# Kernel tuning notes

Hardware: AMD Instinct MI355X
Metric: run time of the kernel (lower is better)

## Reference

```python
import jax, jax.numpy as jnp
import numpy as np

NH, HD, MB = 32, 64, 16        # heads, head_dim, TTT mini-batch size
BASE_LR = 1.0
ROPE_THETA = 10000.0


def _ln(x, w, b, eps):
    mu = x.mean(-1, keepdims=True)
    var = ((x - mu) ** 2).mean(-1, keepdims=True)
    return (x - mu) / jnp.sqrt(var + eps) * w + b


def _rotate_half(x):
    x1, x2 = jnp.split(x, 2, axis=-1)
    return jnp.concatenate([-x2, x1], axis=-1)


def _ln_l2_bwd(x, target, g, b, eps=1e-6):
    # grad of ||LN(x)*g+b - target||^2 / 2 wrt x (fused, as in ttt-lm)
    D = x.shape[-1]
    mu = x.mean(-1, keepdims=True)
    var = ((x - mu) ** 2).mean(-1, keepdims=True)
    std = jnp.sqrt(var + eps)
    xh = (x - mu) / std
    gxh = (g * xh + b - target) * g
    return (D * gxh - gxh.sum(-1, keepdims=True) - xh * (gxh * xh).sum(-1, keepdims=True)) / (D * std)


def _ttt_forward(x, q_w, k_w, v_w, o_w, ttt_lr_w, ttt_lr_b, token_idx_off,
                 ttt_norm_w, ttt_norm_b, W1, b1, post_w, post_b):
    B, L, C = x.shape
    NM = L // MB
    XQ = (x @ q_w).reshape(B, L, NH, HD).transpose(0, 2, 1, 3)  # [B,NH,L,HD]
    XK = (x @ k_w).reshape(B, L, NH, HD).transpose(0, 2, 1, 3)
    XV = (x @ v_w).reshape(B, L, NH, HD).transpose(0, 2, 1, 3)
    # rotary embedding at position_ids % mini_batch_size
    pos = (jnp.arange(L) % MB).astype(jnp.float32)
    inv = 1.0 / (ROPE_THETA ** (jnp.arange(0, HD, 2, dtype=jnp.float32) / HD))
    fr = pos[:, None] * inv[None, :]
    emb = jnp.concatenate([fr, fr], axis=-1)           # [L,HD]
    cos, sin = jnp.cos(emb), jnp.sin(emb)
    XQ = XQ * cos + _rotate_half(XQ) * sin
    XK = XK * cos + _rotate_half(XK) * sin
    # learning-rate gate (eta)
    Xm = x.reshape(B, NM, MB, C)
    ttt_lr = jax.nn.sigmoid(jnp.einsum('bnkc,hdc->bhnkd', Xm, ttt_lr_w)
                            + ttt_lr_b.reshape(1, NH, 1, 1, 1))       # [B,NH,NM,MB,1]
    ttt_lr_eta = BASE_LR * ttt_lr.transpose(0, 1, 2, 4, 3) / HD       # [B,NH,NM,1,MB]
    tok = jnp.maximum(1.0 / jnp.arange(1, MB + 1, dtype=jnp.float32) + token_idx_off, 0.0)
    eta = tok.reshape(1, 1, 1, MB, 1) * ttt_lr_eta                    # [B,NH,NM,MB,MB]

    def tomb(t):  # [B,NH,L,HD] -> [NM,B,NH,MB,HD]
        return t.reshape(B, NH, NM, MB, HD).transpose(2, 0, 1, 3, 4)

    xs = (tomb(XQ), tomb(XK), tomb(XV), eta.transpose(2, 0, 1, 3, 4))
    lw = ttt_norm_w.reshape(1, NH, 1, HD)
    lb = ttt_norm_b.reshape(1, NH, 1, HD)
    tril = jnp.tril(jnp.ones((MB, MB), x.dtype))
    W1s = jnp.broadcast_to(W1, (B, NH, HD, HD)).astype(x.dtype)
    b1s = jnp.broadcast_to(b1, (B, NH, 1, HD)).astype(x.dtype)

    def step(carry, xs_t):
        W1c, b1c = carry
        xq, xk, xv, et = xs_t                      # [B,NH,MB,HD], et [B,NH,MB,MB]
        Z1 = xk @ W1c + b1c
        grad = _ln_l2_bwd(Z1, xv - xk, lw, lb)     # grad of per-head TTT loss wrt Z1
        Attn1 = jnp.tril(xq @ xk.transpose(0, 1, 3, 2))
        b1_bar = b1c - (et * tril) @ grad
        Z1_bar = xq @ W1c - (et * Attn1) @ grad + b1_bar
        last_eta = et[:, :, -1, :, None]           # [B,NH,MB,1]
        W1n = W1c - jnp.einsum('bhki,bhkj->bhij', last_eta * xk, grad)
        b1n = b1c - (last_eta * grad).sum(-2, keepdims=True)
        out = xq + _ln(Z1_bar, lw, lb, 1e-6)
        return (W1n, b1n), out

    _, outs = jax.lax.scan(step, (W1s, b1s), xs)   # outs: [NM,B,NH,MB,HD]
    y = outs.transpose(1, 0, 3, 2, 4).reshape(B, L, C)
    y = _ln(y, post_w, post_b, 1e-6)
    return y @ o_w


def setup_inputs() -> dict:
    key = jax.random.key(0)
    ks = jax.random.split(key, 16)
    B, L, C, DH = 4, 2048, 2048, 1024
    s = 0.02
    return {
        'enc_input': jax.random.normal(ks[0], (B, L, C), jnp.float32),
        'ln1_w': jnp.ones((C,), jnp.float32), 'ln1_b': jnp.zeros((C,), jnp.float32),
        'q_w': jax.random.normal(ks[1], (C, C), jnp.float32) * s,
        'k_w': jax.random.normal(ks[2], (C, C), jnp.float32) * s,
        'v_w': jax.random.normal(ks[3], (C, C), jnp.float32) * s,
        'o_w': jax.random.normal(ks[4], (C, C), jnp.float32) * s,
        'ttt_lr_w': jax.random.normal(ks[5], (NH, 1, C), jnp.float32) * s,
        'ttt_lr_b': jax.random.normal(ks[6], (NH,), jnp.float32) * s,
        'token_idx_off': jax.random.normal(ks[7], (MB,), jnp.float32) * 0.01,
        'ttt_norm_w': jnp.ones((NH, HD), jnp.float32),
        'ttt_norm_b': jnp.zeros((NH, HD), jnp.float32),
        'W1': jax.random.normal(ks[8], (NH, HD, HD), jnp.float32) * s,
        'b1': jnp.zeros((NH, 1, HD), jnp.float32),
        'post_w': jnp.ones((C,), jnp.float32), 'post_b': jnp.zeros((C,), jnp.float32),
        'ffn_ln_w': jnp.ones((C,), jnp.float32), 'ffn_ln_b': jnp.zeros((C,), jnp.float32),
        'w1f': jax.random.normal(ks[9], (C, DH), jnp.float32) * s,
        'b1f': jnp.zeros((DH,), jnp.float32),
        'w2f': jax.random.normal(ks[10], (DH, C), jnp.float32) * s,
        'b2f': jnp.zeros((C,), jnp.float32),
    }


def reference(enc_input, ln1_w, ln1_b, q_w, k_w, v_w, o_w, ttt_lr_w, ttt_lr_b,
              token_idx_off, ttt_norm_w, ttt_norm_b, W1, b1, post_w, post_b,
              ffn_ln_w, ffn_ln_b, w1f, b1f, w2f, b2f):
    # pre-LN (torch default eps=1e-5) + TTT linear block + residual
    x = _ln(enc_input, ln1_w, ln1_b, 1e-5)
    y = _ttt_forward(x, q_w, k_w, v_w, o_w, ttt_lr_w, ttt_lr_b, token_idx_off,
                     ttt_norm_w, ttt_norm_b, W1, b1, post_w, post_b)
    y = y + enc_input
    # position-wise FFN (pre-LN eps=1e-6) + residual; dropout = eval no-op
    z = _ln(y, ffn_ln_w, ffn_ln_b, 1e-6)
    z = jax.nn.relu(z @ w1f + b1f) @ w2f + b2f
    return z + y
```

## Files before the change

### kernel.cpp

```cpp
#include <hip/hip_runtime.h>

typedef unsigned short u16;
typedef __attribute__((ext_vector_type(8))) short short8;
typedef __attribute__((ext_vector_type(8))) unsigned short ushort8;
typedef __attribute__((ext_vector_type(4))) float f32x4;
typedef __attribute__((ext_vector_type(2))) float f32x2;

#define DEV __device__ __forceinline__

DEV float bf2f(u16 u){ union{unsigned int i; float f;} v; v.i = ((unsigned int)u)<<16u; return v.f; }
DEV u16 f2bf(float f){ union{float f; unsigned int i;} v; v.f=f; unsigned int r = v.i + 0x7FFFu + ((v.i>>16)&1u); return (u16)(r>>16); }

DEV void gload16(const u16* g, u16* l){
  __builtin_amdgcn_global_load_lds((const __attribute__((address_space(1))) void*)g,
                                   (__attribute__((address_space(3))) void*)l, 16, 0, 0);
}

DEV float wsum(float v){
  v += __shfl_xor(v, 32, 64);
  v += __shfl_xor(v, 16, 64);
  v += __shfl_xor(v, 8, 64);
  v += __shfl_xor(v, 4, 64);
  v += __shfl_xor(v, 2, 64);
  v += __shfl_xor(v, 1, 64);
  return v;
}
DEV float qsum(float v){
  v += __shfl_xor(v, 16, 64);
  v += __shfl_xor(v, 32, 64);
  return v;
}
DEV float jsum(float v){
  v += __shfl_xor(v, 1, 64);
  v += __shfl_xor(v, 2, 64);
  v += __shfl_xor(v, 4, 64);
  v += __shfl_xor(v, 8, 64);
  return v;
}

DEV float block_sum(float v, float* red){
  v = wsum(v);
  __syncthreads();
  if((threadIdx.x & 63u)==0) red[threadIdx.x>>6] = v;
  __syncthreads();
  return red[0]+red[1]+red[2]+red[3];
}

#define BARS() do{ asm volatile("s_waitcnt lgkmcnt(0)" ::: "memory"); \
  __builtin_amdgcn_s_barrier(); __builtin_amdgcn_sched_barrier(0); }while(0)

__global__ __launch_bounds__(256) void ln_row(
    const float* __restrict__ in, const float* __restrict__ w, const float* __restrict__ bb,
    float eps, u16* __restrict__ outb)
{
  __shared__ float red[4];
  const int row = blockIdx.x, t = threadIdx.x;
  const float* p = in + (size_t)row*2048 + t*8;
  f32x4 a = *(const f32x4*)p;
  f32x4 c = *(const f32x4*)(p+4);
  float s = a[0]+a[1]+a[2]+a[3]+c[0]+c[1]+c[2]+c[3];
  s = block_sum(s, red);
  float mu = s*(1.f/2048.f);
  float vs = 0.f;
  #pragma unroll
  for(int j=0;j<4;j++){ float d=a[j]-mu; vs += d*d; }
  #pragma unroll
  for(int j=0;j<4;j++){ float d=c[j]-mu; vs += d*d; }
  vs = block_sum(vs, red);
  float rstd = rsqrtf(vs*(1.f/2048.f) + eps);
  f32x4 w0 = *(const f32x4*)(w + t*8);
  f32x4 w1 = *(const f32x4*)(w + t*8 + 4);
  f32x4 b0 = *(const f32x4*)(bb + t*8);
  f32x4 b1 = *(const f32x4*)(bb + t*8 + 4);
  ushort8 o;
  #pragma unroll
  for(int j=0;j<4;j++) o[j]   = f2bf((a[j]-mu)*rstd*w0[j] + b0[j]);
  #pragma unroll
  for(int j=0;j<4;j++) o[j+4] = f2bf((c[j]-mu)*rstd*w1[j] + b1[j]);
  *(ushort8*)(outb + (size_t)row*2048 + t*8) = o;
}

__global__ __launch_bounds__(256) void transpose_cast(
    const float* __restrict__ src, u16* __restrict__ dst, int K, int N)
{
  __shared__ float tile[32][33];
  const int kb = blockIdx.x*32, nb = blockIdx.y*32;
  const int tx = threadIdx.x & 31, ty = threadIdx.x >> 5;
  #pragma unroll
  for(int i=0;i<4;i++){
    int k = ty + i*8;
    tile[k][tx] = src[(size_t)(kb+k)*N + nb + tx];
  }
  __syncthreads();
  #pragma unroll
  for(int i=0;i<4;i++){
    int nn = ty + i*8;
    dst[(size_t)(nb+nn)*K + kb + tx] = f2bf(tile[tx][nn]);
  }
}

__global__ __launch_bounds__(256) void cast_lrw(const float* __restrict__ lrw, u16* __restrict__ dst)
{
  int i = blockIdx.x*256 + threadIdx.x;
  if (i < 32*2048) dst[i] = f2bf(lrw[i]);
  else dst[i] = 0;
}

__global__ void rope_init(const float* __restrict__ tio, float* __restrict__ cosb,
                          float* __restrict__ sinb, float* __restrict__ tokb)
{
  int t = blockIdx.x*256 + threadIdx.x;
  if (t < 1024){
    int p = t>>6, d = t&63;
    float inv = powf(10000.f, -(float)(2*(d&31))/64.f);
    float fr = (float)p * inv;
    cosb[t] = cosf(fr);
    sinb[t] = sinf(fr);
  }
  if (blockIdx.x==0 && threadIdx.x<16)
    tokb[threadIdx.x] = fmaxf(1.f/(float)(threadIdx.x+1) + tio[threadIdx.x], 0.f);
}

#define MM(MI,NI,AA,BB) acc[MI][NI] = __builtin_amdgcn_mfma_f32_16x16x32_bf16(AA, BB, acc[MI][NI], 0, 0, 0)

#define RD_A(D,KH,MF) (*(const short8*)(ldsb + ((D)<<16) + ((KH)<<14) + (wm<<13) + ((MF)<<10) + loff))
#define RD_B(D,KH,NF) (*(const short8*)(ldsb + ((D)<<16) + 32768 + ((KH)<<14) + (wn<<12) + ((NF)<<10) + loff))

#define PHASE(D,KH,MH,RB,STG,VM) { \
  __builtin_amdgcn_sched_barrier(0); \
  if (RB){ b0 = RD_B(D,KH,0); b1 = RD_B(D,KH,1); b2 = RD_B(D,KH,2); b3 = RD_B(D,KH,3); } \
  short8 a0 = RD_A(D,KH,4*(MH)+0); \
  short8 a1 = RD_A(D,KH,4*(MH)+1); \
  short8 a2 = RD_A(D,KH,4*(MH)+2); \
  short8 a3 = RD_A(D,KH,4*(MH)+3); \
  STG; \
  __builtin_amdgcn_sched_barrier(0); \
  __builtin_amdgcn_s_barrier(); \
  asm volatile("s_waitcnt lgkmcnt(0)" ::: "memory"); \
  __builtin_amdgcn_sched_barrier(0); \
  __builtin_amdgcn_s_setprio(1); \
  MM(4*(MH)+0,0,a0,b0); MM(4*(MH)+1,0,a1,b0); MM(4*(MH)+2,0,a2,b0); MM(4*(MH)+3,0,a3,b0); \
  MM(4*(MH)+0,1,a0,b1); MM(4*(MH)+1,1,a1,b1); MM(4*(MH)+2,1,a2,b1); MM(4*(MH)+3,1,a3,b1); \
  MM(4*(MH)+0,2,a0,b2); MM(4*(MH)+1,2,a1,b2); MM(4*(MH)+2,2,a2,b2); MM(4*(MH)+3,2,a3,b2); \
  MM(4*(MH)+0,3,a0,b3); MM(4*(MH)+1,3,a1,b3); MM(4*(MH)+2,3,a2,b3); MM(4*(MH)+3,3,a3,b3); \
  __builtin_amdgcn_s_setprio(0); \
  if (VM){ asm volatile("s_waitcnt vmcnt(8)" ::: "memory"); } \
  __builtin_amdgcn_sched_barrier(0); \
  __builtin_amdgcn_s_barrier(); \
}

template<int EPI>
__global__ __launch_bounds__(512, 2) void gemm256(
    const u16* __restrict__ A, const u16* __restrict__ Bt,
    float* __restrict__ C, u16* __restrict__ Cb,
    const float* __restrict__ bias, const float* __restrict__ resid,
    int Nld, int Nreal, int K, int ntN)
{
  extern __shared__ u16 lds[];
  const int t = threadIdx.x, lane = t&63, wv = t>>6;
  const int wm = wv>>2, wn = wv&3;
  const int fr = lane&15, kq = lane>>4;

  int bid = blockIdx.x;
  {
    int nwg = gridDim.x;
    int q = nwg>>3, r = nwg&7;
    int x = bid&7, l = bid>>3;
    bid = (x<r) ? (x*(q+1)+l) : (r*(q+1)+(x-r)*q+l);
  }
  const int bm = bid/ntN, bn = bid%ntN;

  f32x4 acc[8][4];
  #pragma unroll
  for(int i=0;i<8;i++)
    #pragma unroll
    for(int j=0;j<4;j++) acc[i][j]=(f32x4){0.f,0.f,0.f,0.f};

  const u16* gA = A  + (size_t)(bm*256)*K;
  const u16* gB = Bt + (size_t)(bn*256)*K;

  const int Ls   = (t&7) ^ ((t>>3)&7);
  const int rstg = ((t>>3)<<1) | (Ls>>2);
  const int cstg = (Ls&3)<<3;
  u16* const ldsw = lds + (wv<<9);

  const int Plane = (((fr&1)<<2) | kq) ^ (fr>>1);
  const int loff  = ((fr>>1)<<7) | (Plane<<4);
  const char* const ldsb = (const char*)lds;

  auto stA = [&](int d, int kh, int kts){
    u16* lb = ldsw + (d<<15) + (kh<<13);
    const u16* g = gA + (size_t)rstg*K + kts + (kh<<5) + cstg;
    gload16(g, lb);
    gload16(g + ((size_t)K<<7), lb + 4096);
  };
  auto stB = [&](int d, int kh, int kts){
    u16* lb = ldsw + (d<<15) + 16384 + (kh<<13);
    const u16* g = gB + (size_t)rstg*K + kts + (kh<<5) + cstg;
    gload16(g, lb);
    gload16(g + ((size_t)K<<7), lb + 4096);
  };

  stA(0,0,0); stB(0,0,0); stA(0,1,0); stB(0,1,0); stA(1,0,64); stB(1,0,64);
  asm volatile("s_waitcnt vmcnt(8)" ::: "memory");
  __builtin_amdgcn_sched_barrier(0);
  __builtin_amdgcn_s_barrier();

  for (int kt = 0; kt < K; kt += 128){
    const int ktp = (kt+128 < K) ? kt+128 : 0;
    const int ktq = (kt+192 < K) ? kt+192 : kt+192-K;
    short8 b0={0},b1={0},b2={0},b3={0};
    PHASE(0,0,0,1, stA(1,1,kt+64), 0)
    PHASE(0,0,1,0, stB(1,1,kt+64), 1)
    PHASE(0,1,0,1, stA(0,0,ktp),   0)
    PHASE(0,1,1,0, stB(0,0,ktp),   1)
    PHASE(1,0,0,1, stA(0,1,ktp),   0)
    PHASE(1,0,1,0, stB(0,1,ktp),   1)
    PHASE(1,1,0,1, stA(1,0,ktq),   0)
    PHASE(1,1,1,0, stB(1,0,ktq),   1)
  }

  const int cr = (lane>>4)<<2, cc = lane&15;
  #pragma unroll
  for(int mi=0;mi<8;mi++){
    #pragma unroll
    for(int ni=0;ni<4;ni++){
      const int row0 = bm*256 + wm*128 + mi*16 + cr;
      const int col  = bn*256 + wn*64  + ni*16 + cc;
      if (col < Nreal){
        #pragma unroll
        for(int rr=0;rr<4;rr++){
          size_t idx = (size_t)(row0+rr)*Nld + col;
          float v = acc[mi][ni][rr];
          if (EPI==1 || EPI==3) v += resid[idx];
          if (EPI==2 || EPI==3) v += bias[col];
          if (EPI==2){ v = fmaxf(v, 0.f); Cb[idx] = f2bf(v); }
          else if (EPI==4){ Cb[idx] = f2bf(v); }
          else C[idx] = v;
        }
      }
    }
  }
}

#define W1LD 72
#define XLD  72
#define GTLD 40
#define EKLD 40
#define EALD 40
#define TLD  17

__global__ __launch_bounds__(512, 1) void ttt_scan(
    const u16* __restrict__ XQKV,
    const float* __restrict__ ropec, const float* __restrict__ ropes,
    const float* __restrict__ tokp,
    const float* __restrict__ nw, const float* __restrict__ nb,
    const float* __restrict__ lrb,
    const float* __restrict__ W1i,
    const float* __restrict__ b1i,
    float* __restrict__ Y)
{
  const int blk = blockIdx.x, b = blk>>5, h = blk&31;
  const int t = threadIdx.x, lane = t&63, wv = t>>6;
  const int fr = lane&15, quad = lane>>4;
  const int i0 = wv*2, i1 = i0+1;

  __shared__ u16 W1bf[64*W1LD];
  __shared__ u16 xqbf[2][16*XLD];
  __shared__ u16 xkbf[2][16*XLD];
  __shared__ u16 exkT[2][64*EKLD];
  __shared__ u16 gradTbf[64*GTLD];
  __shared__ u16 etaA[16*EALD];
  __shared__ float tgT[2][64*TLD];
  __shared__ float xqT[2][64*TLD];
  __shared__ float b1s[64];
  __shared__ f32x2 lwlb[64];
  __shared__ float lrs[2][16];
  __shared__ float tokl[16];

  const float lrbh = lrb[h];
  const float cc0 = ropec[i0*64 + lane], ss0 = ropes[i0*64 + lane];
  const float cc1 = ropec[i1*64 + lane], ss1 = ropes[i1*64 + lane];
  const float tok15 = tokp[15];
  const float ct = tok15*(1.f/64.f);
  const float sg = (lane<32)? -1.f : 1.f;

  const int m0 = (wv*2)>>2,   n0 = (wv*2)&3;
  const int m1 = (wv*2+1)>>2, n1 = (wv*2+1)&3;
  f32x4 wfa, wfb;
  {
    const float* wsrc = W1i + (size_t)h*4096;
    #pragma unroll
    for(int r=0;r<4;r++){
      wfa[r] = wsrc[(n0*16+fr)*64 + (m0*16+quad*4+r)];
      wfb[r] = wsrc[(n1*16+fr)*64 + (m1*16+quad*4+r)];
    }
    #pragma unroll
    for(int r=0;r<4;r++){
      W1bf[(m0*16+quad*4+r)*W1LD + n0*16 + fr] = f2bf(wfa[r]);
      W1bf[(m1*16+quad*4+r)*W1LD + n1*16 + fr] = f2bf(wfb[r]);
    }
  }
  for(int i=t;i<64*24;i+=512){
    int rr=i/24, cp=16+i%24;
    gradTbf[rr*GTLD+cp]=0; exkT[0][rr*EKLD+cp]=0; exkT[1][rr*EKLD+cp]=0;
  }
  for(int i=t;i<16*24;i+=512){ int rr=i/24, cp=16+i%24; etaA[rr*EALD+cp]=0; }
  if (t<64){ b1s[t]=b1i[h*64+t]; lwlb[t]=(f32x2){nw[h*64+t], nb[h*64+t]}; }
  if (t<16) tokl[t]=tokp[t];

  auto stage = [&](int bf, u16 Pq0,u16 Pk0,u16 Pv0,u16 Pl0,
                           u16 Pq1,u16 Pk1,u16 Pv1,u16 Pl1){
    float q0=bf2f(Pq0), k0=bf2f(Pk0), v0=bf2f(Pv0);
    float q1=bf2f(Pq1), k1=bf2f(Pk1), v1=bf2f(Pv1);
    float qr0 = q0*cc0 + sg*__shfl_xor(q0,32,64)*ss0;
    float kr0 = k0*cc0 + sg*__shfl_xor(k0,32,64)*ss0;
    float qr1 = q1*cc1 + sg*__shfl_xor(q1,32,64)*ss1;
    float kr1 = k1*cc1 + sg*__shfl_xor(k1,32,64)*ss1;
    float lr0 = 1.f/(1.f + expf(-(bf2f(Pl0) + lrbh)));
    float lr1 = 1.f/(1.f + expf(-(bf2f(Pl1) + lrbh)));
    xqbf[bf][i0*XLD+lane] = f2bf(qr0);
    xqbf[bf][i1*XLD+lane] = f2bf(qr1);
    xkbf[bf][i0*XLD+lane] = f2bf(kr0);
    xkbf[bf][i1*XLD+lane] = f2bf(kr1);
    exkT[bf][lane*EKLD+i0] = f2bf(-ct*lr0*kr0);
    exkT[bf][lane*EKLD+i1] = f2bf(-ct*lr1*kr1);
    tgT[bf][lane*TLD+i0] = v0 - kr0;
    tgT[bf][lane*TLD+i1] = v1 - kr1;
    xqT[bf][lane*TLD+i0] = qr0;
    xqT[bf][lane*TLD+i1] = qr1;
    if (lane==0){ lrs[bf][i0]=lr0; lrs[bf][i1]=lr1; }
  };

  {
    const size_t rb = (size_t)b*2048;
    const u16* p0 = XQKV + (rb+i0)*6272 + h*64 + lane;
    const u16* p1 = XQKV + (rb+i1)*6272 + h*64 + lane;
    u16 l0 = XQKV[(rb+i0)*6272 + 6144 + h];
    u16 l1 = XQKV[(rb+i1)*6272 + 6144 + h];
    stage(0, p0[0],p0[2048],p0[4096],l0, p1[0],p1[2048],p1[4096],l1);
  }
  __syncthreads();

  const f32x4 fzero = (f32x4){0.f,0.f,0.f,0.f};

  for(int n=0;n<128;n++){
    const int cur = n&1, nxt = cur^1;
    const size_t rbase = (size_t)b*2048 + n*16;

    u16 Pq0=0,Pk0=0,Pv0=0,Pl0=0,Pq1=0,Pk1=0,Pv1=0,Pl1=0;
    if (n<127){
      const size_t rb2 = rbase + 16;
      const u16* p0 = XQKV + (rb2+i0)*6272 + h*64 + lane;
      const u16* p1 = XQKV + (rb2+i1)*6272 + h*64 + lane;
      Pq0=p0[0]; Pk0=p0[2048]; Pv0=p0[4096];
      Pq1=p1[0]; Pk1=p1[2048]; Pv1=p1[4096];
      Pl0=XQKV[(rb2+i0)*6272 + 6144 + h];
      Pl1=XQKV[(rb2+i1)*6272 + 6144 + h];
    }

    f32x4 del = fzero;
    f32x4 zq0, zq1, zq2, zq3;
    f32x4 b1q0, b1q1, b1q2, b1q3;
    zq0=zq1=zq2=zq3=fzero; b1q0=b1q1=b1q2=b1q3=fzero;

    if (wv < 4){
      short8 bk0 = *(const short8*)&xkbf[cur][fr*XLD + quad*8];
      short8 bk1 = *(const short8*)&xkbf[cur][fr*XLD + 32 + quad*8];
      f32x4 z0,z1,z2,z3;
      z0 = __builtin_amdgcn_mfma_f32_16x16x32_bf16(*(const short8*)&W1bf[( 0+fr)*W1LD + quad*8],      bk0, fzero, 0,0,0);
      z0 = __builtin_amdgcn_mfma_f32_16x16x32_bf16(*(const short8*)&W1bf[( 0+fr)*W1LD + 32 + quad*8], bk1, z0,    0,0,0);
      z1 = __builtin_amdgcn_mfma_f32_16x16x32_bf16(*(const short8*)&W1bf[(16+fr)*W1LD + quad*8],      bk0, fzero, 0,0,0);
      z1 = __builtin_amdgcn_mfma_f32_16x16x32_bf16(*(const short8*)&W1bf[(16+fr)*W1LD + 32 + quad*8], bk1, z1,    0,0,0);
      z2 = __builtin_amdgcn_mfma_f32_16x16x32_bf16(*(const short8*)&W1bf[(32+fr)*W1LD + quad*8],      bk0, fzero, 0,0,0);
      z2 = __builtin_amdgcn_mfma_f32_16x16x32_bf16(*(const short8*)&W1bf[(32+fr)*W1LD + 32 + quad*8], bk1, z2,    0,0,0);
      z3 = __builtin_amdgcn_mfma_f32_16x16x32_bf16(*(const short8*)&W1bf[(48+fr)*W1LD + quad*8],      bk0, fzero, 0,0,0);
      z3 = __builtin_amdgcn_mfma_f32_16x16x32_bf16(*(const short8*)&W1bf[(48+fr)*W1LD + 32 + quad*8], bk1, z3,    0,0,0);
      f32x4 xh0,xh1,xh2,xh3;
      {
        float s1=0.f, s2=0.f;
        #pragma unroll
        for(int r=0;r<4;r++){
          z0[r] += b1s[ 0+quad*4+r];
          z1[r] += b1s[16+quad*4+r];
          z2[r] += b1s[32+quad*4+r];
          z3[r] += b1s[48+quad*4+r];
          s1 += z0[r]+z1[r]+z2[r]+z3[r];
          s2 += z0[r]*z0[r]+z1[r]*z1[r]+z2[r]*z2[r]+z3[r]*z3[r];
        }
        s1 = qsum(s1); s2 = qsum(s2);
        float mu = s1*(1.f/64.f);
        float var = s2*(1.f/64.f) - mu*mu;
        float rstd = rsqrtf(var + 1e-6f);
        float u1=0.f, u2=0.f;
        #pragma unroll
        for(int m=0;m<4;m++){
          f32x4* zp = (m==0)?&z0:(m==1)?&z1:(m==2)?&z2:&z3;
          f32x4* xp = (m==0)?&xh0:(m==1)?&xh1:(m==2)?&xh2:&xh3;
          #pragma unroll
          for(int r=0;r<4;r++){
            int d = m*16 + quad*4 + r;
            f32x2 wb = lwlb[d];
            float xh = ((*zp)[r] - mu)*rstd;
            float gx = (wb[0]*xh + wb[1] - tgT[cur][d*TLD + fr])*wb[0];
            (*xp)[r] = xh;
            (*zp)[r] = gx;
            u1 += gx; u2 += gx*xh;
          }
        }
        u1 = qsum(u1); u2 = qsum(u2);
        const float c64 = rstd*(1.f/64.f);
        #pragma unroll
        for(int m=0;m<4;m++){
          f32x4* zp = (m==0)?&z0:(m==1)?&z1:(m==2)?&z2:&z3;
          f32x4* xp = (m==0)?&xh0:(m==1)?&xh1:(m==2)?&xh2:&xh3;
          #pragma unroll
          for(int r=0;r<4;r++)
            (*zp)[r] = (64.f*(*zp)[r] - u1 - (*xp)[r]*u2)*c64;
        }
      }
      f32x4 zsel = (wv==0)?z0:(wv==1)?z1:(wv==2)?z2:z3;
      #pragma unroll
      for(int r=0;r<4;r++)
        gradTbf[(wv*16+quad*4+r)*GTLD + fr] = f2bf(zsel[r]);
      float ej = ct * lrs[cur][fr];
      #pragma unroll
      for(int r=0;r<4;r++)
        del[r] = jsum(ej * zsel[r]);
    }
    else if (wv == 4){
      short8 bq0 = *(const short8*)&xqbf[cur][fr*XLD + quad*8];
      short8 bq1 = *(const short8*)&xqbf[cur][fr*XLD + 32 + quad*8];
      zq0 = __builtin_amdgcn_mfma_f32_16x16x32_bf16(*(const short8*)&W1bf[( 0+fr)*W1LD + quad*8],      bq0, fzero, 0,0,0);
      zq0 = __builtin_amdgcn_mfma_f32_16x16x32_bf16(*(const short8*)&W1bf[( 0+fr)*W1LD + 32 + quad*8], bq1, zq0,   0,0,0);
      zq1 = __builtin_amdgcn_mfma_f32_16x16x32_bf16(*(const short8*)&W1bf[(16+fr)*W1LD + quad*8],      bq0, fzero, 0,0,0);
      zq1 = __builtin_amdgcn_mfma_f32_16x16x32_bf16(*(const short8*)&W1bf[(16+fr)*W1LD + 32 + quad*8], bq1, zq1,   0,0,0);
      zq2 = __builtin_amdgcn_mfma_f32_16x16x32_bf16(*(const short8*)&W1bf[(32+fr)*W1LD + quad*8],      bq0, fzero, 0,0,0);
      zq2 = __builtin_amdgcn_mfma_f32_16x16x32_bf16(*(const short8*)&W1bf[(32+fr)*W1LD + 32 + quad*8], bq1, zq2,   0,0,0);
      zq3 = __builtin_amdgcn_mfma_f32_16x16x32_bf16(*(const short8*)&W1bf[(48+fr)*W1LD + quad*8],      bq0, fzero, 0,0,0);
      zq3 = __builtin_amdgcn_mfma_f32_16x16x32_bf16(*(const short8*)&W1bf[(48+fr)*W1LD + 32 + quad*8], bq1, zq3,   0,0,0);
      b1q0 = *(const f32x4*)&b1s[ 0+quad*4];
      b1q1 = *(const f32x4*)&b1s[16+quad*4];
      b1q2 = *(const f32x4*)&b1s[32+quad*4];
      b1q3 = *(const f32x4*)&b1s[48+quad*4];
    }
    else if (wv == 7){
      short8 aq0 = *(const short8*)&xqbf[cur][fr*XLD + quad*8];
      short8 aq1 = *(const short8*)&xqbf[cur][fr*XLD + 32 + quad*8];
      short8 bk0 = *(const short8*)&xkbf[cur][fr*XLD + quad*8];
      short8 bk1 = *(const short8*)&xkbf[cur][fr*XLD + 32 + quad*8];
      f32x4 at;
      at = __builtin_amdgcn_mfma_f32_16x16x32_bf16(aq0, bk0, fzero, 0,0,0);
      at = __builtin_amdgcn_mfma_f32_16x16x32_bf16(aq1, bk1, at,    0,0,0);
      float lrj = lrs[cur][fr]*(1.f/64.f);
      #pragma unroll
      for(int r=0;r<4;r++){
        int i = quad*4 + r;
        float val = (fr <= i) ? -tokl[i]*lrj*(1.f + at[r]) : 0.f;
        etaA[i*EALD + fr] = f2bf(val);
      }
    }
    BARS();

    {
      short8 ga = *(const short8*)&gradTbf[(m0*16+fr)*GTLD + quad*8];
      short8 eb = *(const short8*)&exkT[cur][(n0*16+fr)*EKLD + quad*8];
      wfa = __builtin_amdgcn_mfma_f32_16x16x32_bf16(ga, eb, wfa, 0,0,0);
      short8 gb = *(const short8*)&gradTbf[(m1*16+fr)*GTLD + quad*8];
      short8 eb2 = *(const short8*)&exkT[cur][(n1*16+fr)*EKLD + quad*8];
      wfb = __builtin_amdgcn_mfma_f32_16x16x32_bf16(gb, eb2, wfb, 0,0,0);
      #pragma unroll
      for(int r=0;r<4;r++){
        W1bf[(m0*16+quad*4+r)*W1LD + n0*16 + fr] = f2bf(wfa[r]);
        W1bf[(m1*16+quad*4+r)*W1LD + n1*16 + fr] = f2bf(wfb[r]);
      }
    }
    if (wv == 4){
      short8 be = *(const short8*)&etaA[fr*EALD + quad*8];
      f32x4 c20,c21,c22,c23;
      c20 = __builtin_amdgcn_mfma_f32_16x16x32_bf16(*(const short8*)&gradTbf[( 0+fr)*GTLD + quad*8], be, fzero, 0,0,0);
      c21 = __builtin_amdgcn_mfma_f32_16x16x32_bf16(*(const short8*)&gradTbf[(16+fr)*GTLD + quad*8], be, fzero, 0,0,0);
      c22 = __builtin_amdgcn_mfma_f32_16x16x32_bf16(*(const short8*)&gradTbf[(32+fr)*GTLD + quad*8], be, fzero, 0,0,0);
      c23 = __builtin_amdgcn_mfma_f32_16x16x32_bf16(*(const short8*)&gradTbf[(48+fr)*GTLD + quad*8], be, fzero, 0,0,0);
      f32x4 zb0,zb1,zb2,zb3;
      float s1=0.f, s2=0.f;
      #pragma unroll
      for(int r=0;r<4;r++){
        zb0[r] = zq0[r] + b1q0[r] + c20[r];
        zb1[r] = zq1[r] + b1q1[r] + c21[r];
        zb2[r] = zq2[r] + b1q2[r] + c22[r];
        zb3[r] = zq3[r] + b1q3[r] + c23[r];
        s1 += zb0[r]+zb1[r]+zb2[r]+zb3[r];
        s2 += zb0[r]*zb0[r]+zb1[r]*zb1[r]+zb2[r]*zb2[r]+zb3[r]*zb3[r];
      }
      s1 = qsum(s1); s2 = qsum(s2);
      float mu = s1*(1.f/64.f);
      float var = s2*(1.f/64.f) - mu*mu;
      float rstd = rsqrtf(var + 1e-6f);
      #pragma unroll
      for(int m=0;m<4;m++){
        f32x4* zp = (m==0)?&zb0:(m==1)?&zb1:(m==2)?&zb2:&zb3;
        #pragma unroll
        for(int r=0;r<4;r++){
          int d = m*16 + quad*4 + r;
          f32x2 wb = lwlb[d];
          float xh = ((*zp)[r] - mu)*rstd;
          Y[(rbase+fr)*2048 + h*64 + d] = xqT[cur][d*TLD + fr] + xh*wb[0] + wb[1];
        }
      }
    }
    if (wv < 4 && fr == 0){
      #pragma unroll
      for(int r=0;r<4;r++) b1s[wv*16+quad*4+r] -= del[r];
    }
    if (n<127) stage(nxt, Pq0,Pk0,Pv0,Pl0, Pq1,Pk1,Pv1,Pl1);
    BARS();
  }
}

extern "C" void kernel_launch(void* const* d_in, const int* in_sizes, int n_in,
                              void* d_out, int out_size, void* d_ws, size_t ws_size,
                              hipStream_t stream)
{
  const float* enc   = (const float*)d_in[0];
  const float* ln1w  = (const float*)d_in[1];
  const float* ln1b  = (const float*)d_in[2];
  const float* qw    = (const float*)d_in[3];
  const float* kw    = (const float*)d_in[4];
  const float* vw    = (const float*)d_in[5];
  const float* ow    = (const float*)d_in[6];
  const float* lrw   = (const float*)d_in[7];
  const float* lrb   = (const float*)d_in[8];
  const float* tio   = (const float*)d_in[9];
  const float* tnw   = (const float*)d_in[10];
  const float* tnb   = (const float*)d_in[11];
  const float* W1i   = (const float*)d_in[12];
  const float* b1i   = (const float*)d_in[13];
  const float* postw = (const float*)d_in[14];
  const float* postb = (const float*)d_in[15];
  const float* flnw  = (const float*)d_in[16];
  const float* flnb  = (const float*)d_in[17];
  const float* w1f   = (const float*)d_in[18];
  const float* b1f   = (const float*)d_in[19];
  const float* w2f   = (const float*)d_in[20];
  const float* b2f   = (const float*)d_in[21];
  float* out = (float*)d_out;

  char* ws = (char*)d_ws;
  size_t off = 0;
  auto alloc = [&](size_t bytes)->void*{ void* p = ws + off; off += (bytes + 255) & ~(size_t)255; return p; };
  u16*   regA  = (u16*)  alloc(8192ull*2048*2);
  u16*   wqkvT = (u16*)  alloc(6400ull*2048*2);
  u16*   XQKV  = (u16*)  alloc(8192ull*6272*2);
  float* yb    = (float*)alloc(8192ull*2048*4);
  float* ropec = (float*)alloc(1024*4);
  float* ropes = (float*)alloc(1024*4);
  float* tokb  = (float*)alloc(64*4);

  u16* oT   = wqkvT;
  u16* w1fT = wqkvT + 2048ull*2048;
  u16* w2fT = w1fT + 1024ull*2048;
  u16* hbf  = XQKV;
  float* y2 = yb;

  static bool s_attr = false;
  if (!s_attr){
    s_attr = true;
    (void)hipFuncSetAttribute(reinterpret_cast<const void*>(gemm256<4>), hipFuncAttributeMaxDynamicSharedMemorySize, 131072);
    (void)hipFuncSetAttribute(reinterpret_cast<const void*>(gemm256<1>), hipFuncAttributeMaxDynamicSharedMemorySize, 131072);
    (void)hipFuncSetAttribute(reinterpret_cast<const void*>(gemm256<2>), hipFuncAttributeMaxDynamicSharedMemorySize, 131072);
    (void)hipFuncSetAttribute(reinterpret_cast<const void*>(gemm256<3>), hipFuncAttributeMaxDynamicSharedMemorySize, 131072);
  }

  rope_init<<<4, 256, 0, stream>>>(tio, ropec, ropes, tokb);

  dim3 tg1(64, 64);
  transpose_cast<<<tg1, 256, 0, stream>>>(qw, wqkvT,               2048, 2048);
  transpose_cast<<<tg1, 256, 0, stream>>>(kw, wqkvT + 2048ull*2048, 2048, 2048);
  transpose_cast<<<tg1, 256, 0, stream>>>(vw, wqkvT + 4096ull*2048, 2048, 2048);
  cast_lrw<<<2048, 256, 0, stream>>>(lrw, wqkvT + 6144ull*2048);

  ln_row<<<8192, 256, 0, stream>>>(enc, ln1w, ln1b, 1e-5f, regA);

  gemm256<4><<<32*25, 512, 131072, stream>>>(regA, wqkvT, nullptr, XQKV,
                                             nullptr, nullptr, 6272, 6272, 2048, 25);

  transpose_cast<<<tg1, 256, 0, stream>>>(ow, oT, 2048, 2048);
  dim3 tg2(64, 32);
  transpose_cast<<<tg2, 256, 0, stream>>>(w1f, w1fT, 2048, 1024);
  dim3 tg3(32, 64);
  transpose_cast<<<tg3, 256, 0, stream>>>(w2f, w2fT, 1024, 2048);

  ttt_scan<<<128, 512, 0, stream>>>(XQKV, ropec, ropes, tokb, tnw, tnb, lrb, W1i, b1i, yb);

  ln_row<<<8192, 256, 0, stream>>>(yb, postw, postb, 1e-6f, regA);
  gemm256<1><<<32*8, 512, 131072, stream>>>(regA, oT, y2, nullptr,
                                            nullptr, enc, 2048, 2048, 2048, 8);

  ln_row<<<8192, 256, 0, stream>>>(y2, flnw, flnb, 1e-6f, regA);
  gemm256<2><<<32*4, 512, 131072, stream>>>(regA, w1fT, nullptr, hbf,
                                            b1f, nullptr, 1024, 1024, 2048, 4);
  gemm256<3><<<32*8, 512, 131072, stream>>>(hbf, w2fT, out, nullptr,
                                            b2f, y2, 2048, 2048, 1024, 8);
}
```

Before: 886.6 us.

## Move W1 update into gradient waves with double-buffered W1 and offload b1 update

Waves 0-3 now apply the W1 update right after writing their own gradient rows, each keeping a full 16-row W1 slab in registers and writing it into a double-buffered bf16 W1 copy. This removes the W1 update phase that all eight waves ran after the barrier. The b1 update moves from per-wave jsum reductions to wave 5, which reads the bf16 gradient from shared memory, so b1 loses some precision. Smaller changes: qsum uses permlane swaps when the builtins exist, tgT, xqT and layer-norm weights are preloaded into registers, and Y is written with vector stores.

Measured after the change: 857.1 us. 1.03x faster.

```diff
diff --git a/kernel.cpp b/kernel.cpp
--- a/kernel.cpp
+++ b/kernel.cpp
@@ -5,6 +5,7 @@
 typedef __attribute__((ext_vector_type(8))) unsigned short ushort8;
 typedef __attribute__((ext_vector_type(4))) float f32x4;
 typedef __attribute__((ext_vector_type(2))) float f32x2;
+typedef __attribute__((ext_vector_type(2))) unsigned int uint2v;
 
 #define DEV __device__ __forceinline__
 
@@ -25,18 +26,23 @@
   v += __shfl_xor(v, 1, 64);
   return v;
 }
+
+#if __has_builtin(__builtin_amdgcn_permlane16_swap) && __has_builtin(__builtin_amdgcn_permlane32_swap)
+DEV float qsum(float v){
+  unsigned u = __float_as_uint(v);
+  uint2v a = __builtin_amdgcn_permlane16_swap(u, u, false, false);
+  float s = __uint_as_float(a[0]) + __uint_as_float(a[1]);
+  unsigned u2 = __float_as_uint(s);
+  uint2v bsw = __builtin_amdgcn_permlane32_swap(u2, u2, false, false);
+  return __uint_as_float(bsw[0]) + __uint_as_float(bsw[1]);
+}
+#else
 DEV float qsum(float v){
   v += __shfl_xor(v, 16, 64);
   v += __shfl_xor(v, 32, 64);
   return v;
 }
-DEV float jsum(float v){
-  v += __shfl_xor(v, 1, 64);
-  v += __shfl_xor(v, 2, 64);
-  v += __shfl_xor(v, 4, 64);
-  v += __shfl_xor(v, 8, 64);
-  return v;
-}
+#endif
 
 DEV float block_sum(float v, float* red){
   v = wsum(v);
@@ -265,7 +271,7 @@
   const int fr = lane&15, quad = lane>>4;
   const int i0 = wv*2, i1 = i0+1;
 
-  __shared__ u16 W1bf[64*W1LD];
+  __shared__ u16 W1bf[2][64*W1LD];
   __shared__ u16 xqbf[2][16*XLD];
   __shared__ u16 xkbf[2][16*XLD];
   __shared__ u16 exkT[2][64*EKLD];
@@ -285,20 +291,24 @@
   const float ct = tok15*(1.f/64.f);
   const float sg = (lane<32)? -1.f : 1.f;
 
-  const int m0 = (wv*2)>>2,   n0 = (wv*2)&3;
-  const int m1 = (wv*2+1)>>2, n1 = (wv*2+1)&3;
-  f32x4 wfa, wfb;
-  {
+  f32x4 wf0, wf1, wf2, wf3;
+  if (wv < 4){
     const float* wsrc = W1i + (size_t)h*4096;
     #pragma unroll
     for(int r=0;r<4;r++){
-      wfa[r] = wsrc[(n0*16+fr)*64 + (m0*16+quad*4+r)];
-      wfb[r] = wsrc[(n1*16+fr)*64 + (m1*16+quad*4+r)];
+      int d = wv*16+quad*4+r;
+      wf0[r] = wsrc[( 0+fr)*64 + d];
+      wf1[r] = wsrc[(16+fr)*64 + d];
+      wf2[r] = wsrc[(32+fr)*64 + d];
+      wf3[r] = wsrc[(48+fr)*64 + d];
     }
     #pragma unroll
     for(int r=0;r<4;r++){
-      W1bf[(m0*16+quad*4+r)*W1LD + n0*16 + fr] = f2bf(wfa[r]);
-      W1bf[(m1*16+quad*4+r)*W1LD + n1*16 + fr] = f2bf(wfb[r]);
+      int d = wv*16+quad*4+r;
+      W1bf[0][d*W1LD +  0 + fr] = f2bf(wf0[r]);
+      W1bf[0][d*W1LD + 16 + fr] = f2bf(wf1[r]);
+      W1bf[0][d*W1LD + 32 + fr] = f2bf(wf2[r]);
+      W1bf[0][d*W1LD + 48 + fr] = f2bf(wf3[r]);
     }
   }
   for(int i=t;i<64*24;i+=512){
@@ -346,6 +356,7 @@
 
   for(int n=0;n<128;n++){
     const int cur = n&1, nxt = cur^1;
+    const int cb = n&1, nbuf = cb^1;
     const size_t rbase = (size_t)b*2048 + n*16;
 
     u16 Pq0=0,Pk0=0,Pv0=0,Pl0=0,Pq1=0,Pk1=0,Pv1=0,Pl1=0;
@@ -359,32 +370,46 @@
       Pl1=XQKV[(rb2+i1)*6272 + 6144 + h];
     }
 
-    f32x4 del = fzero;
     f32x4 zq0, zq1, zq2, zq3;
     f32x4 b1q0, b1q1, b1q2, b1q3;
+    float xq_r[16];
+    f32x2 lw4[16];
     zq0=zq1=zq2=zq3=fzero; b1q0=b1q1=b1q2=b1q3=fzero;
 
     if (wv < 4){
+      f32x4 b1v0 = *(const f32x4*)&b1s[ 0+quad*4];
+      f32x4 b1v1 = *(const f32x4*)&b1s[16+quad*4];
+      f32x4 b1v2 = *(const f32x4*)&b1s[32+quad*4];
+      f32x4 b1v3 = *(const f32x4*)&b1s[48+quad*4];
+      float tg[16]; f32x2 lwv[16];
+      #pragma unroll
+      for(int m=0;m<4;m++)
+        #pragma unroll
+        for(int r=0;r<4;r++){
+          int d = m*16+quad*4+r;
+          tg[m*4+r]  = tgT[cur][d*TLD + fr];
+          lwv[m*4+r] = lwlb[d];
+        }
       short8 bk0 = *(const short8*)&xkbf[cur][fr*XLD + quad*8];
       short8 bk1 = *(const short8*)&xkbf[cur][fr*XLD + 32 + quad*8];
       f32x4 z0,z1,z2,z3;
-      z0 = __builtin_amdgcn_mfma_f32_16x16x32_bf16(*(const short8*)&W1bf[( 0+fr)*W1LD + quad*8],      bk0, fzero, 0,0,0);
-      z0 = __builtin_amdgcn_mfma_f32_16x16x32_bf16(*(const short8*)&W1bf[( 0+fr)*W1LD + 32 + quad*8], bk1, z0,    0,0,0);
-      z1 = __builtin_amdgcn_mfma_f32_16x16x32_bf16(*(const short8*)&W1bf[(16+fr)*W1LD + quad*8],      bk0, fzero, 0,0,0);
-      z1 = __builtin_amdgcn_mfma_f32_16x16x32_bf16(*(const short8*)&W1bf[(16+fr)*W1LD + 32 + quad*8], bk1, z1,    0,0,0);
-      z2 = __builtin_amdgcn_mfma_f32_16x16x32_bf16(*(const short8*)&W1bf[(32+fr)*W1LD + quad*8],      bk0, fzero, 0,0,0);
-      z2 = __builtin_amdgcn_mfma_f32_16x16x32_bf16(*(const short8*)&W1bf[(32+fr)*W1LD + 32 + quad*8], bk1, z2,    0,0,0);
-      z3 = __builtin_amdgcn_mfma_f32_16x16x32_bf16(*(const short8*)&W1bf[(48+fr)*W1LD + quad*8],      bk0, fzero, 0,0,0);
-      z3 = __builtin_amdgcn_mfma_f32_16x16x32_bf16(*(const short8*)&W1bf[(48+fr)*W1LD + 32 + quad*8], bk1, z3,    0,0,0);
+      z0 = __builtin_amdgcn_mfma_f32_16x16x32_bf16(*(const short8*)&W1bf[cb][( 0+fr)*W1LD + quad*8],      bk0, fzero, 0,0,0);
+      z0 = __builtin_amdgcn_mfma_f32_16x16x32_bf16(*(const short8*)&W1bf[cb][( 0+fr)*W1LD + 32 + quad*8], bk1, z0,    0,0,0);
+      z1 = __builtin_amdgcn_mfma_f32_16x16x32_bf16(*(const short8*)&W1bf[cb][(16+fr)*W1LD + quad*8],      bk0, fzero, 0,0,0);
+      z1 = __builtin_amdgcn_mfma_f32_16x16x32_bf16(*(const short8*)&W1bf[cb][(16+fr)*W1LD + 32 + quad*8], bk1, z1,    0,0,0);
+      z2 = __builtin_amdgcn_mfma_f32_16x16x32_bf16(*(const short8*)&W1bf[cb][(32+fr)*W1LD + quad*8],      bk0, fzero, 0,0,0);
+      z2 = __builtin_amdgcn_mfma_f32_16x16x32_bf16(*(const short8*)&W1bf[cb][(32+fr)*W1LD + 32 + quad*8], bk1, z2,    0,0,0);
+      z3 = __builtin_amdgcn_mfma_f32_16x16x32_bf16(*(const short8*)&W1bf[cb][(48+fr)*W1LD + quad*8],      bk0, fzero, 0,0,0);
+      z3 = __builtin_amdgcn_mfma_f32_16x16x32_bf16(*(const short8*)&W1bf[cb][(48+fr)*W1LD + 32 + quad*8], bk1, z3,    0,0,0);
       f32x4 xh0,xh1,xh2,xh3;
       {
         float s1=0.f, s2=0.f;
         #pragma unroll
         for(int r=0;r<4;r++){
-          z0[r] += b1s[ 0+quad*4+r];
-          z1[r] += b1s[16+quad*4+r];
-          z2[r] += b1s[32+quad*4+r];
-          z3[r] += b1s[48+quad*4+r];
+          z0[r] += b1v0[r];
+          z1[r] += b1v1[r];
+          z2[r] += b1v2[r];
+          z3[r] += b1v3[r];
           s1 += z0[r]+z1[r]+z2[r]+z3[r];
           s2 += z0[r]*z0[r]+z1[r]*z1[r]+z2[r]*z2[r]+z3[r]*z3[r];
         }
@@ -399,10 +424,9 @@
           f32x4* xp = (m==0)?&xh0:(m==1)?&xh1:(m==2)?&xh2:&xh3;
           #pragma unroll
           for(int r=0;r<4;r++){
-            int d = m*16 + quad*4 + r;
-            f32x2 wb = lwlb[d];
+            f32x2 wb = lwv[m*4+r];
             float xh = ((*zp)[r] - mu)*rstd;
-            float gx = (wb[0]*xh + wb[1] - tgT[cur][d*TLD + fr])*wb[0];
+            float gx = (wb[0]*xh + wb[1] - tg[m*4+r])*wb[0];
             (*xp)[r] = xh;
             (*zp)[r] = gx;
             u1 += gx; u2 += gx*xh;
@@ -423,26 +447,48 @@
       #pragma unroll
       for(int r=0;r<4;r++)
         gradTbf[(wv*16+quad*4+r)*GTLD + fr] = f2bf(zsel[r]);
-      float ej = ct * lrs[cur][fr];
-      #pragma unroll
-      for(int r=0;r<4;r++)
-        del[r] = jsum(ej * zsel[r]);
+      asm volatile("s_waitcnt lgkmcnt(0)" ::: "memory");
+      short8 ga = *(const short8*)&gradTbf[(wv*16+fr)*GTLD + quad*8];
+      short8 e0 = *(const short8*)&exkT[cur][( 0+fr)*EKLD + quad*8];
+      short8 e1 = *(const short8*)&exkT[cur][(16+fr)*EKLD + quad*8];
+      short8 e2 = *(const short8*)&exkT[cur][(32+fr)*EKLD + quad*8];
+      short8 e3 = *(const short8*)&exkT[cur][(48+fr)*EKLD + quad*8];
+      wf0 = __builtin_amdgcn_mfma_f32_16x16x32_bf16(ga, e0, wf0, 0,0,0);
+      wf1 = __builtin_amdgcn_mfma_f32_16x16x32_bf16(ga, e1, wf1, 0,0,0);
+      wf2 = __builtin_amdgcn_mfma_f32_16x16x32_bf16(ga, e2, wf2, 0,0,0);
+      wf3 = __builtin_amdgcn_mfma_f32_16x16x32_bf16(ga, e3, wf3, 0,0,0);
+      #pragma unroll
+      for(int r=0;r<4;r++){
+        int d = wv*16+quad*4+r;
+        W1bf[nbuf][d*W1LD +  0 + fr] = f2bf(wf0[r]);
+        W1bf[nbuf][d*W1LD + 16 + fr] = f2bf(wf1[r]);
+        W1bf[nbuf][d*W1LD + 32 + fr] = f2bf(wf2[r]);
+        W1bf[nbuf][d*W1LD + 48 + fr] = f2bf(wf3[r]);
+      }
     }
     else if (wv == 4){
-      short8 bq0 = *(const short8*)&xqbf[cur][fr*XLD + quad*8];
-      short8 bq1 = *(const short8*)&xqbf[cur][fr*XLD + 32 + quad*8];
-      zq0 = __builtin_amdgcn_mfma_f32_16x16x32_bf16(*(const short8*)&W1bf[( 0+fr)*W1LD + quad*8],      bq0, fzero, 0,0,0);
-      zq0 = __builtin_amdgcn_mfma_f32_16x16x32_bf16(*(const short8*)&W1bf[( 0+fr)*W1LD + 32 + quad*8], bq1, zq0,   0,0,0);
-      zq1 = __builtin_amdgcn_mfma_f32_16x16x32_bf16(*(const short8*)&W1bf[(16+fr)*W1LD + quad*8],      bq0, fzero, 0,0,0);
-      zq1 = __builtin_amdgcn_mfma_f32_16x16x32_bf16(*(const short8*)&W1bf[(16+fr)*W1LD + 32 + quad*8], bq1, zq1,   0,0,0);
-      zq2 = __builtin_amdgcn_mfma_f32_16x16x32_bf16(*(const short8*)&W1bf[(32+fr)*W1LD + quad*8],      bq0, fzero, 0,0,0);
-      zq2 = __builtin_amdgcn_mfma_f32_16x16x32_bf16(*(const short8*)&W1bf[(32+fr)*W1LD + 32 + quad*8], bq1, zq2,   0,0,0);
-      zq3 = __builtin_amdgcn_mfma_f32_16x16x32_bf16(*(const short8*)&W1bf[(48+fr)*W1LD + quad*8],      bq0, fzero, 0,0,0);
-      zq3 = __builtin_amdgcn_mfma_f32_16x16x32_bf16(*(const short8*)&W1bf[(48+fr)*W1LD + 32 + quad*8], bq1, zq3,   0,0,0);
       b1q0 = *(const f32x4*)&b1s[ 0+quad*4];
       b1q1 = *(const f32x4*)&b1s[16+quad*4];
       b1q2 = *(const f32x4*)&b1s[32+quad*4];
       b1q3 = *(const f32x4*)&b1s[48+quad*4];
+      #pragma unroll
+      for(int m=0;m<4;m++)
+        #pragma unroll
+        for(int r=0;r<4;r++){
+          int d = m*16+quad*4+r;
+          xq_r[m*4+r] = xqT[cur][d*TLD + fr];
+          lw4[m*4+r]  = lwlb[d];
+        }
+      short8 bq0 = *(const short8*)&xqbf[cur][fr*XLD + quad*8];
+      short8 bq1 = *(const short8*)&xqbf[cur][fr*XLD + 32 + quad*8];
+      zq0 = __builtin_amdgcn_mfma_f32_16x16x32_bf16(*(const short8*)&W1bf[cb][( 0+fr)*W1LD + quad*8],      bq0, fzero, 0,0,0);
+      zq0 = __builtin_amdgcn_mfma_f32_16x16x32_bf16(*(const short8*)&W1bf[cb][( 0+fr)*W1LD + 32 + quad*8], bq1, zq0,   0,0,0);
+      zq1 = __builtin_amdgcn_mfma_f32_16x16x32_bf16(*(const short8*)&W1bf[cb][(16+fr)*W1LD + quad*8],      bq0, fzero, 0,0,0);
+      zq1 = __builtin_amdgcn_mfma_f32_16x16x32_bf16(*(const short8*)&W1bf[cb][(16+fr)*W1LD + 32 + quad*8], bq1, zq1,   0,0,0);
+      zq2 = __builtin_amdgcn_mfma_f32_16x16x32_bf16(*(const short8*)&W1bf[cb][(32+fr)*W1LD + quad*8],      bq0, fzero, 0,0,0);
+      zq2 = __builtin_amdgcn_mfma_f32_16x16x32_bf16(*(const short8*)&W1bf[cb][(32+fr)*W1LD + 32 + quad*8], bq1, zq2,   0,0,0);
+      zq3 = __builtin_amdgcn_mfma_f32_16x16x32_bf16(*(const short8*)&W1bf[cb][(48+fr)*W1LD + quad*8],      bq0, fzero, 0,0,0);
+      zq3 = __builtin_amdgcn_mfma_f32_16x16x32_bf16(*(const short8*)&W1bf[cb][(48+fr)*W1LD + 32 + quad*8], bq1, zq3,   0,0,0);
     }
     else if (wv == 7){
       short8 aq0 = *(const short8*)&xqbf[cur][fr*XLD + quad*8];
@@ -462,19 +508,6 @@
     }
     BARS();
 
-    {
-      short8 ga = *(const short8*)&gradTbf[(m0*16+fr)*GTLD + quad*8];
-      short8 eb = *(const short8*)&exkT[cur][(n0*16+fr)*EKLD + quad*8];
-      wfa = __builtin_amdgcn_mfma_f32_16x16x32_bf16(ga, eb, wfa, 0,0,0);
-      short8 gb = *(const short8*)&gradTbf[(m1*16+fr)*GTLD + quad*8];
-      short8 eb2 = *(const short8*)&exkT[cur][(n1*16+fr)*EKLD + quad*8];
-      wfb = __builtin_amdgcn_mfma_f32_16x16x32_bf16(gb, eb2, wfb, 0,0,0);
-      #pragma unroll
-      for(int r=0;r<4;r++){
-        W1bf[(m0*16+quad*4+r)*W1LD + n0*16 + fr] = f2bf(wfa[r]);
-        W1bf[(m1*16+quad*4+r)*W1LD + n1*16 + fr] = f2bf(wfb[r]);
-      }
-    }
     if (wv == 4){
       short8 be = *(const short8*)&etaA[fr*EALD + quad*8];
       f32x4 c20,c21,c22,c23;
@@ -500,18 +533,26 @@
       #pragma unroll
       for(int m=0;m<4;m++){
         f32x4* zp = (m==0)?&zb0:(m==1)?&zb1:(m==2)?&zb2:&zb3;
+        f32x4 o;
         #pragma unroll
         for(int r=0;r<4;r++){
-          int d = m*16 + quad*4 + r;
-          f32x2 wb = lwlb[d];
+          f32x2 wb = lw4[m*4+r];
           float xh = ((*zp)[r] - mu)*rstd;
-          Y[(rbase+fr)*2048 + h*64 + d] = xqT[cur][d*TLD + fr] + xh*wb[0] + wb[1];
+          o[r] = xq_r[m*4+r] + xh*wb[0] + wb[1];
         }
+        *(f32x4*)&Y[(rbase+fr)*2048 + h*64 + m*16 + quad*4] = o;
       }
     }
-    if (wv < 4 && fr == 0){
-      #pragma unroll
-      for(int r=0;r<4;r++) b1s[wv*16+quad*4+r] -= del[r];
+    else if (wv == 5){
+      const int d = lane;
+      short8 g0 = *(const short8*)&gradTbf[d*GTLD + 0];
+      short8 g1 = *(const short8*)&gradTbf[d*GTLD + 8];
+      float s = 0.f;
+      #pragma unroll
+      for(int j=0;j<8;j++) s += lrs[cur][j]   * bf2f((u16)g0[j]);
+      #pragma unroll
+      for(int j=0;j<8;j++) s += lrs[cur][8+j] * bf2f((u16)g1[j]);
+      b1s[d] -= ct * s;
     }
     if (n<127) stage(nxt, Pq0,Pk0,Pv0,Pl0, Pq1,Pk1,Pv1,Pl1);
     BARS();
```
